# Performance work log

Measured on AMD Instinct MI355X. Metric: run time of the kernel, lower is better.

## Reference

```python
import jax, jax.numpy as jnp
import numpy as np

N, D, B = 8192, 512, 64
EPS = 1e-5


def _layernorm(x, w, b):
    mu = jnp.mean(x, axis=-1, keepdims=True)
    var = jnp.mean(jnp.square(x - mu), axis=-1, keepdims=True)
    return (x - mu) * jax.lax.rsqrt(var + EPS) * w + b


def setup_inputs() -> dict:
    key = jax.random.key(0)
    ks = jax.random.split(key, 10)
    s = 0.02
    return {
        "x_mole": jax.random.normal(ks[0], (N, D), jnp.float32),
        "x_conf": jax.random.normal(ks[1], (N, D), jnp.float32),
        "W1": jax.random.normal(ks[2], (D, D), jnp.float32) * s,   # attention_1 (no bias)
        "W2": jax.random.normal(ks[3], (D, D), jnp.float32) * s,   # attention_2 (no bias)
        "phi1_w": jnp.ones((D,), jnp.float32),
        "phi1_b": jnp.zeros((D,), jnp.float32),
        "phi2_w": jnp.ones((D,), jnp.float32),
        "phi2_b": jnp.zeros((D,), jnp.float32),
        "rho_w1": jax.random.normal(ks[4], (D, D), jnp.float32) * s,
        "rho_b1": jnp.zeros((D,), jnp.float32),
        "rho_w2": jax.random.normal(ks[5], (D, D), jnp.float32) * s,
        "rho_b2": jnp.zeros((D,), jnp.float32),
        "rho_ln_w": jnp.ones((D,), jnp.float32),
        "rho_ln_b": jnp.zeros((D,), jnp.float32),
        "batch": jnp.sort(jax.random.randint(ks[6], (N,), 0, B, jnp.int64)),
    }


def reference(x_mole, x_conf, W1, W2, phi1_w, phi1_b, phi2_w, phi2_b,
              rho_w1, rho_b1, rho_w2, rho_b2, rho_ln_w, rho_ln_b, batch):
    # projections of LayerNormed inputs (torch Linear: y = x @ W^T)
    q = _layernorm(x_mole, phi1_w, phi1_b) @ W1.T          # [N, D]
    k = _layernorm(x_conf, phi2_w, phi2_b) @ W2.T          # [N, D]
    dot = q @ k.T                                          # [N, N]

    # block-diagonal batch-equality mask and hand-rolled masked softmax
    mask = (batch[:, None] == batch[None, :]).astype(dot.dtype)  # [N, N]
    max_values = jnp.max(dot * mask, axis=1, keepdims=True)
    masked = (dot - max_values) * mask
    e = jnp.exp(masked)
    attn = e / jnp.sum(e * mask, axis=1, keepdims=True)
    attn = attn * mask                                     # [N, N]

    x_weighted = attn @ x_conf                             # [N, D]

    # rho MLP: Linear -> SiLU -> Linear -> SiLU -> LayerNorm
    h = jax.nn.silu(x_weighted @ rho_w1.T + rho_b1)
    h = jax.nn.silu(h @ rho_w2.T + rho_b2)
    x_encoded = _layernorm(h, rho_ln_w, rho_ln_b)
    return x_encoded, attn
```

## Files before the change

kernel.cpp:

```cpp
#include <hip/hip_runtime.h>

namespace {

constexpr int N = 8192;
constexpr int D = 512;
constexpr int NBATCH = 64;
constexpr int SEGMAX = 256;
constexpr int XCW = NBATCH * SEGMAX;
constexpr size_t MB = 1u << 20;

using s16x8 = __attribute__((ext_vector_type(8))) short;
using f32x4 = __attribute__((ext_vector_type(4))) float;

__device__ inline short f2bf(float f) {
  unsigned u = __float_as_uint(f);
  u += 0x7fffu + ((u >> 16) & 1u);
  return (short)(u >> 16);
}
__device__ inline float bf2f(short h) {
  return __uint_as_float(((unsigned)(unsigned short)h) << 16);
}
__device__ inline void split2(float f, short& hi, short& lo) {
  hi = f2bf(f);
  lo = f2bf(f - bf2f(hi));
}

__device__ inline f32x4 mfma16(s16x8 a, s16x8 b, f32x4 c) {
  return __builtin_amdgcn_mfma_f32_16x16x32_bf16(a, b, c, 0, 0, 0);
}

__device__ inline void gl16(const short* g, short* l) {
  __builtin_amdgcn_global_load_lds((const __attribute__((address_space(1))) void*)g,
                                   (__attribute__((address_space(3))) void*)l, 16, 0, 0);
}

__device__ inline void ln_row(const float* __restrict__ x, const float* __restrict__ w,
                              const float* __restrict__ bsrc, int row, int lane,
                              float o[8]) {
  const float* xr = x + (size_t)row * D + lane * 8;
  f32x4 v0 = *(const f32x4*)xr;
  f32x4 v1 = *(const f32x4*)(xr + 4);
  float s = 0.f, sq = 0.f;
#pragma unroll
  for (int j = 0; j < 4; j++) {
    s += v0[j] + v1[j];
    sq += v0[j] * v0[j] + v1[j] * v1[j];
  }
#pragma unroll
  for (int off = 32; off >= 1; off >>= 1) {
    s += __shfl_xor(s, off);
    sq += __shfl_xor(sq, off);
  }
  float mu = s * (1.f / D);
  float var = sq * (1.f / D) - mu * mu;
  float rs = rsqrtf(var + 1e-5f);
  const float* wp = w + lane * 8;
  const float* bp = bsrc + lane * 8;
  f32x4 w0 = *(const f32x4*)wp, w1 = *(const f32x4*)(wp + 4);
  f32x4 b0 = *(const f32x4*)bp, b1 = *(const f32x4*)(bp + 4);
#pragma unroll
  for (int j = 0; j < 4; j++) {
    o[j] = (v0[j] - mu) * rs * w0[j] + b0[j];
    o[j + 4] = (v1[j] - mu) * rs * w1[j] + b1[j];
  }
}

__global__ __launch_bounds__(256) void ln_split2(
    const float* __restrict__ x0, const float* __restrict__ w0,
    const float* __restrict__ b0, short* __restrict__ oh0, short* __restrict__ ol0,
    const float* __restrict__ x1, const float* __restrict__ w1,
    const float* __restrict__ b1, short* __restrict__ oh1, short* __restrict__ ol1) {
  const float* x = blockIdx.y ? x1 : x0;
  const float* w = blockIdx.y ? w1 : w0;
  const float* b = blockIdx.y ? b1 : b0;
  short* oh = blockIdx.y ? oh1 : oh0;
  short* ol = blockIdx.y ? ol1 : ol0;
  int row = blockIdx.x * 4 + (threadIdx.x >> 6);
  int lane = threadIdx.x & 63;
  float o[8];
  ln_row(x, w, b, row, lane, o);
  s16x8 hi, lo;
#pragma unroll
  for (int j = 0; j < 8; j++) {
    short h, l;
    split2(o[j], h, l);
    hi[j] = h; lo[j] = l;
  }
  *(s16x8*)(oh + (size_t)row * D + lane * 8) = hi;
  *(s16x8*)(ol + (size_t)row * D + lane * 8) = lo;
}

__global__ __launch_bounds__(256) void ln_f32(const float* __restrict__ x,
                                              const float* __restrict__ w,
                                              const float* __restrict__ bsrc,
                                              float* __restrict__ out) {
  int row = blockIdx.x * 4 + (threadIdx.x >> 6);
  int lane = threadIdx.x & 63;
  float o[8];
  ln_row(x, w, bsrc, row, lane, o);
  f32x4 o0, o1;
#pragma unroll
  for (int j = 0; j < 4; j++) { o0[j] = o[j]; o1[j] = o[j + 4]; }
  float* op = out + (size_t)row * D + lane * 8;
  *(f32x4*)op = o0;
  *(f32x4*)(op + 4) = o1;
}

__global__ __launch_bounds__(256) void castsplit4(
    const float* __restrict__ s0, const float* __restrict__ s1,
    const float* __restrict__ s2, const float* __restrict__ s3,
    short* __restrict__ h0, short* __restrict__ l0,
    short* __restrict__ h1, short* __restrict__ l1,
    short* __restrict__ h2, short* __restrict__ l2,
    short* __restrict__ h3, short* __restrict__ l3) {
  const float* s; short* h; short* l;
  switch (blockIdx.y) {
    case 0: s = s0; h = h0; l = l0; break;
    case 1: s = s1; h = h1; l = l1; break;
    case 2: s = s2; h = h2; l = l2; break;
    default: s = s3; h = h3; l = l3; break;
  }
  int i = blockIdx.x * 256 + threadIdx.x;
  f32x4 a = *(const f32x4*)(s + (size_t)i * 8);
  f32x4 b = *(const f32x4*)(s + (size_t)i * 8 + 4);
  s16x8 oh, ol;
#pragma unroll
  for (int j = 0; j < 4; j++) {
    short hh, ll;
    split2(a[j], hh, ll); oh[j] = hh; ol[j] = ll;
    split2(b[j], hh, ll); oh[j + 4] = hh; ol[j + 4] = ll;
  }
  *(s16x8*)(h + (size_t)i * 8) = oh;
  *(s16x8*)(l + (size_t)i * 8) = ol;
}

__global__ void seg_kernel(const int* __restrict__ batch, int* __restrict__ seg,
                           int* __restrict__ colmap) {
  int stride = (batch[N - 1] == 0) ? 2 : 1;
  int t = threadIdx.x;
  if (t <= NBATCH) {
    int lo = 0, hi = N;
    while (lo < hi) {
      int mid = (lo + hi) >> 1;
      if (batch[mid * stride] < t) lo = mid + 1; else hi = mid;
    }
    seg[t] = lo;
  }
  __syncthreads();
  for (int r = t; r < N; r += 256) {
    int bb = batch[r * stride];
    colmap[r] = bb * SEGMAX + (r - seg[bb]);
  }
}

__global__ __launch_bounds__(256) void transpose_xc(const float* __restrict__ xc,
                                                    const int* __restrict__ colmap,
                                                    short* __restrict__ xcT) {
  __shared__ float tile[32][33];
  int tx = threadIdx.x & 31, ty = threadIdx.x >> 5;
  int r0 = blockIdx.x * 32, c0 = blockIdx.y * 32;
#pragma unroll
  for (int p = 0; p < 4; p++)
    tile[ty + p * 8][tx] = xc[(size_t)(r0 + ty + p * 8) * D + c0 + tx];
  __syncthreads();
  int cp = colmap[r0 + tx];
#pragma unroll
  for (int p = 0; p < 4; p++) {
    int d = c0 + ty + p * 8;
    xcT[(size_t)d * XCW + cp] = f2bf(tile[tx][ty + p * 8]);
  }
}

template <int SPLITA, int EPI>
__global__ __launch_bounds__(256) void gemm_lds(const short* __restrict__ Ahi,
                                                const short* __restrict__ Alo,
                                                const short* __restrict__ Bhi,
                                                const short* __restrict__ Blo,
                                                const float* __restrict__ bias,
                                                void* __restrict__ C0,
                                                void* __restrict__ C1) {
  constexpr int ASZ = 64 * 32;
  constexpr int BSZ = 128 * 32;
  constexpr int AH = 0;
  constexpr int AL = ASZ;
  constexpr int BH = SPLITA ? 2 * ASZ : ASZ;
  constexpr int BL = BH + BSZ;
  constexpr int STEP = BL + BSZ;
  __shared__ short lds[2][STEP];

  int tid = threadIdx.x;
  int w = tid >> 6, l = tid & 63, lr = l & 15, kg = l >> 4;
  int wm = w >> 1, wn = w & 1;

  int o = blockIdx.y * 4 + blockIdx.x;
  int xcd = o & 7, slot = o >> 3;
  int by = xcd * 16 + (slot >> 2);
  int bx = slot & 3;
  int m_base = by * 64;
  int n_base = bx * 128;

  int srow = tid >> 2;
  int gch = (tid & 3) ^ ((tid >> 3) & 3);
  const short* a_h = Ahi + (size_t)(m_base + srow) * D + gch * 8;
  const short* a_l = SPLITA ? (Alo + (size_t)(m_base + srow) * D + gch * 8) : nullptr;
  const short* b_h = Bhi + (size_t)(n_base + srow) * D + gch * 8;
  const short* b_l = Blo + (size_t)(n_base + srow) * D + gch * 8;

  int aoff[2], boff[4];
#pragma unroll
  for (int fo = 0; fo < 2; fo++) {
    int row = wm * 32 + fo * 16 + lr;
    aoff[fo] = row * 32 + ((kg ^ ((row >> 1) & 3)) << 3);
  }
#pragma unroll
  for (int fo = 0; fo < 4; fo++) {
    int row = wn * 64 + fo * 16 + lr;
    boff[fo] = row * 32 + ((kg ^ ((row >> 1) & 3)) << 3);
  }

  f32x4 acc[2][4] = {};

  auto STAGE = [&](int c, int ko) {
    gl16(a_h + ko, &lds[c][AH + w * 512]);
    if (SPLITA) gl16(a_l + ko, &lds[c][AL + w * 512]);
    gl16(b_h + ko, &lds[c][BH + w * 512]);
    gl16(b_h + (size_t)64 * D + ko, &lds[c][BH + 2048 + w * 512]);
    gl16(b_l + ko, &lds[c][BL + w * 512]);
    gl16(b_l + (size_t)64 * D + ko, &lds[c][BL + 2048 + w * 512]);
  };

  STAGE(0, 0);
  __syncthreads();
#pragma unroll
  for (int s = 0; s < 16; ++s) {
    int cur = s & 1;
    if (s < 15) STAGE(cur ^ 1, (s + 1) * 32);
    s16x8 av[2], alv[2], bv[4], blv[4];
#pragma unroll
    for (int i = 0; i < 2; i++) {
      av[i] = *(const s16x8*)&lds[cur][AH + aoff[i]];
      if (SPLITA) alv[i] = *(const s16x8*)&lds[cur][AL + aoff[i]];
    }
#pragma unroll
    for (int j = 0; j < 4; j++) {
      bv[j] = *(const s16x8*)&lds[cur][BH + boff[j]];
      blv[j] = *(const s16x8*)&lds[cur][BL + boff[j]];
    }
#pragma unroll
    for (int i = 0; i < 2; i++)
#pragma unroll
      for (int j = 0; j < 4; j++) {
        if (SPLITA)
          acc[i][j] = mfma16(av[i], bv[j],
                             mfma16(av[i], blv[j], mfma16(alv[i], bv[j], acc[i][j])));
        else
          acc[i][j] = mfma16(av[i], bv[j], mfma16(av[i], blv[j], acc[i][j]));
      }
    __syncthreads();
  }

#pragma unroll
  for (int i = 0; i < 2; i++)
#pragma unroll
    for (int j = 0; j < 4; j++) {
      int col = n_base + wn * 64 + j * 16 + lr;
      float bv2 = (EPI >= 1) ? bias[col] : 0.f;
#pragma unroll
      for (int r = 0; r < 4; r++) {
        int rowg = m_base + wm * 32 + i * 16 + kg * 4 + r;
        float v = acc[i][j][r];
        if (EPI >= 1) { v += bv2; v = v / (1.f + __expf(-v)); }
        if (EPI == 0) {
          short h, lo2;
          split2(v, h, lo2);
          ((short*)C0)[(size_t)rowg * D + col] = h;
          ((short*)C1)[(size_t)rowg * D + col] = lo2;
        } else if (EPI == 1) {
          ((short*)C0)[(size_t)rowg * D + col] = f2bf(v);
        } else {
          ((float*)C0)[(size_t)rowg * D + col] = v;
        }
      }
    }
}

__global__ __launch_bounds__(256) void attn_kernel(const short* __restrict__ qh,
                                                   const short* __restrict__ ql,
                                                   const short* __restrict__ kh,
                                                   const short* __restrict__ kl,
                                                   const short* __restrict__ xcT,
                                                   const int* __restrict__ seg,
                                                   float* __restrict__ attn_out,
                                                   short* __restrict__ xw) {
  __shared__ float Ss[32][260];
  __shared__ short Ph[32][256];
  int b = blockIdx.y;
  int s0 = seg[b];
  int nb = seg[b + 1] - s0;
  int r0 = blockIdx.x * 32;
  if (r0 >= nb) return;
  int tid = threadIdx.x;
  int w = tid >> 6, l = tid & 63, lr = l & 15, kg = l >> 4;
  int row8 = tid >> 3, sub = tid & 7;
  bool rvalid = (r0 + row8) < nb;

  size_t q0 = (size_t)(s0 + r0 + lr) * D + kg * 8;
  size_t q1 = q0 + 16 * D;
  int ncf = (nb + 15) >> 4;
  for (int f = w; f < ncf; f += 4) {
    f32x4 a0 = {0, 0, 0, 0}, a1 = {0, 0, 0, 0};
    size_t kr = (size_t)(s0 + f * 16 + lr) * D + kg * 8;
    for (int k0 = 0; k0 < D; k0 += 32) {
      s16x8 kH = *(const s16x8*)(kh + kr + k0);
      s16x8 kL = *(const s16x8*)(kl + kr + k0);
      s16x8 qH0 = *(const s16x8*)(qh + q0 + k0);
      s16x8 qH1 = *(const s16x8*)(qh + q1 + k0);
      s16x8 qL0 = *(const s16x8*)(ql + q0 + k0);
      s16x8 qL1 = *(const s16x8*)(ql + q1 + k0);
      a0 = mfma16(qH0, kH, mfma16(qH0, kL, mfma16(qL0, kH, a0)));
      a1 = mfma16(qH1, kH, mfma16(qH1, kL, mfma16(qL1, kH, a1)));
    }
#pragma unroll
    for (int r = 0; r < 4; r++) {
      Ss[kg * 4 + r][f * 16 + lr] = a0[r];
      Ss[16 + kg * 4 + r][f * 16 + lr] = a1[r];
    }
  }
  __syncthreads();

  int nbp32 = (nb + 31) & ~31;
  if (rvalid) {
    float m = 0.f;
    for (int j = sub; j < nb; j += 8) m = fmaxf(m, Ss[row8][j]);
    m = fmaxf(m, __shfl_xor(m, 1));
    m = fmaxf(m, __shfl_xor(m, 2));
    m = fmaxf(m, __shfl_xor(m, 4));
    float sum = 0.f;
    for (int j = sub; j < nb; j += 8) {
      float e = __expf(Ss[row8][j] - m);
      Ss[row8][j] = e;
      sum += e;
    }
    sum += __shfl_xor(sum, 1);
    sum += __shfl_xor(sum, 2);
    sum += __shfl_xor(sum, 4);
    float inv = 1.f / sum;
    float* orow = attn_out + (size_t)(s0 + r0 + row8) * N + s0;
    for (int j = sub; j < nbp32; j += 8) {
      int sw = ((((j >> 3) ^ (row8 & 7)) << 3) | (j & 7));
      if (j < nb) {
        float a = Ss[row8][j] * inv;
        orow[j] = a;
        Ph[row8][sw] = f2bf(a);
      } else {
        Ph[row8][sw] = 0;
      }
    }
  }
  __syncthreads();

  for (int f2 = w * 8; f2 < w * 8 + 8; f2++) {
    f32x4 a0 = {0, 0, 0, 0}, a1 = {0, 0, 0, 0};
    const short* xrow = xcT + (size_t)(f2 * 16 + lr) * XCW + b * SEGMAX + kg * 8;
    for (int j0 = 0; j0 < nbp32; j0 += 32) {
      int ch = (j0 >> 3) + kg;
      int swo = ((ch ^ (lr & 7)) << 3);
      s16x8 pH0 = *(const s16x8*)&Ph[lr][swo];
      s16x8 pH1 = *(const s16x8*)&Ph[16 + lr][swo];
      s16x8 xv = *(const s16x8*)(xrow + j0);
      a0 = mfma16(pH0, xv, a0);
      a1 = mfma16(pH1, xv, a1);
    }
#pragma unroll
    for (int r = 0; r < 4; r++) {
      int rr0 = kg * 4 + r, rr1 = 16 + kg * 4 + r;
      if (r0 + rr0 < nb) xw[(size_t)(s0 + r0 + rr0) * D + f2 * 16 + lr] = f2bf(a0[r]);
      if (r0 + rr1 < nb) xw[(size_t)(s0 + r0 + rr1) * D + f2 * 16 + lr] = f2bf(a1[r]);
    }
  }
}

}

extern "C" void kernel_launch(void* const* d_in, const int* in_sizes, int n_in,
                              void* d_out, int out_size, void* d_ws, size_t ws_size,
                              hipStream_t stream) {
  (void)in_sizes; (void)n_in; (void)out_size; (void)ws_size;
  const float* x_mole = (const float*)d_in[0];
  const float* x_conf = (const float*)d_in[1];
  const float* W1 = (const float*)d_in[2];
  const float* W2 = (const float*)d_in[3];
  const float* phi1_w = (const float*)d_in[4];
  const float* phi1_b = (const float*)d_in[5];
  const float* phi2_w = (const float*)d_in[6];
  const float* phi2_b = (const float*)d_in[7];
  const float* rho_w1 = (const float*)d_in[8];
  const float* rho_b1 = (const float*)d_in[9];
  const float* rho_w2 = (const float*)d_in[10];
  const float* rho_b2 = (const float*)d_in[11];
  const float* rho_ln_w = (const float*)d_in[12];
  const float* rho_ln_b = (const float*)d_in[13];
  const int* batch = (const int*)d_in[14];

  float* out = (float*)d_out;
  float* attn_out = out + (size_t)N * D;

  char* w8 = (char*)d_ws;
  short* xm_hi = (short*)(w8 + 0 * MB);
  short* xm_lo = (short*)(w8 + 8 * MB);
  short* xc_hi = (short*)(w8 + 16 * MB);
  short* xc_lo = (short*)(w8 + 24 * MB);
  short* q_hi  = (short*)(w8 + 32 * MB);
  short* q_lo  = (short*)(w8 + 41 * MB);
  short* k_hi  = (short*)(w8 + 50 * MB);
  short* k_lo  = (short*)(w8 + 59 * MB);
  short* xcT   = (short*)(w8 + 68 * MB);
  short* w1h   = (short*)(w8 + 84 * MB);
  short* w1l   = (short*)(w8 + 84 * MB + 524288);
  short* w2h   = (short*)(w8 + 85 * MB);
  short* w2l   = (short*)(w8 + 85 * MB + 524288);
  short* r1h   = (short*)(w8 + 86 * MB);
  short* r1l   = (short*)(w8 + 86 * MB + 524288);
  short* r2h   = (short*)(w8 + 87 * MB);
  short* r2l   = (short*)(w8 + 87 * MB + 524288);
  int*   seg   = (int*)(w8 + 88 * MB);
  int*   colmap = (int*)(w8 + 88 * MB + 512);
  float* h2    = (float*)(w8 + 32 * MB);
  short* xw = xm_hi;
  short* h1 = xc_hi;

  hipMemsetAsync((void*)attn_out, 0, (size_t)N * N * sizeof(float), stream);

  seg_kernel<<<1, 256, 0, stream>>>(batch, seg, colmap);
  castsplit4<<<dim3(128, 4), 256, 0, stream>>>(W1, W2, rho_w1, rho_w2,
                                               w1h, w1l, w2h, w2l,
                                               r1h, r1l, r2h, r2l);
  ln_split2<<<dim3(N / 4, 2), 256, 0, stream>>>(x_mole, phi1_w, phi1_b, xm_hi, xm_lo,
                                                x_conf, phi2_w, phi2_b, xc_hi, xc_lo);
  transpose_xc<<<dim3(N / 32, D / 32), 256, 0, stream>>>(x_conf, colmap, xcT);
  gemm_lds<1, 0><<<dim3(4, 128), 256, 0, stream>>>(xm_hi, xm_lo, w1h, w1l, nullptr,
                                                   q_hi, q_lo);
  gemm_lds<1, 0><<<dim3(4, 128), 256, 0, stream>>>(xc_hi, xc_lo, w2h, w2l, nullptr,
                                                   k_hi, k_lo);
  attn_kernel<<<dim3(SEGMAX / 32, NBATCH), 256, 0, stream>>>(q_hi, q_lo, k_hi, k_lo,
                                                             xcT, seg, attn_out, xw);
  gemm_lds<0, 1><<<dim3(4, 128), 256, 0, stream>>>(xw, nullptr, r1h, r1l, rho_b1,
                                                   h1, nullptr);
  gemm_lds<0, 2><<<dim3(4, 128), 256, 0, stream>>>(h1, nullptr, r2h, r2l, rho_b2,
                                                   h2, nullptr);
  ln_f32<<<N / 4, 256, 0, stream>>>(h2, rho_ln_w, rho_ln_b, out);
}
```

Baseline: 515.3 us.

## Fuse prep kernels, batch QK projections, and deepen GEMM prefetch pipeline

Merges the layernorm-split, weight cast-split and segment-index kernels into one launch, and runs the Q and K projection GEMMs as one grid with a z dimension. The GEMM main loop now keeps two stages in flight, using explicit vmcnt waits and raw barriers instead of a full syncthreads per step. This is meant to cut launch overhead and hide global-to-LDS latency, at the cost of more fragile manual synchronization.

```diff
diff --git a/kernel.cpp b/kernel.cpp
--- a/kernel.cpp
+++ b/kernel.cpp
@@ -32,6 +32,11 @@
 __device__ inline void gl16(const short* g, short* l) {
   __builtin_amdgcn_global_load_lds((const __attribute__((address_space(1))) void*)g,
                                    (__attribute__((address_space(3))) void*)l, 16, 0, 0);
+}
+
+template <int Nn>
+__device__ inline void vmw() {
+  asm volatile("s_waitcnt vmcnt(%0)" ::"i"(Nn) : "memory");
 }
 
 __device__ inline void ln_row(const float* __restrict__ x, const float* __restrict__ w,
@@ -65,29 +70,75 @@
   }
 }
 
-__global__ __launch_bounds__(256) void ln_split2(
-    const float* __restrict__ x0, const float* __restrict__ w0,
-    const float* __restrict__ b0, short* __restrict__ oh0, short* __restrict__ ol0,
-    const float* __restrict__ x1, const float* __restrict__ w1,
-    const float* __restrict__ b1, short* __restrict__ oh1, short* __restrict__ ol1) {
-  const float* x = blockIdx.y ? x1 : x0;
-  const float* w = blockIdx.y ? w1 : w0;
-  const float* b = blockIdx.y ? b1 : b0;
-  short* oh = blockIdx.y ? oh1 : oh0;
-  short* ol = blockIdx.y ? ol1 : ol0;
-  int row = blockIdx.x * 4 + (threadIdx.x >> 6);
-  int lane = threadIdx.x & 63;
-  float o[8];
-  ln_row(x, w, b, row, lane, o);
-  s16x8 hi, lo;
-#pragma unroll
-  for (int j = 0; j < 8; j++) {
-    short h, l;
-    split2(o[j], h, l);
-    hi[j] = h; lo[j] = l;
-  }
-  *(s16x8*)(oh + (size_t)row * D + lane * 8) = hi;
-  *(s16x8*)(ol + (size_t)row * D + lane * 8) = lo;
+__global__ __launch_bounds__(256) void prep_kernel(
+    const float* __restrict__ x_mole, const float* __restrict__ phi1_w,
+    const float* __restrict__ phi1_b, short* __restrict__ xm_hi, short* __restrict__ xm_lo,
+    const float* __restrict__ x_conf, const float* __restrict__ phi2_w,
+    const float* __restrict__ phi2_b, short* __restrict__ xc_hi, short* __restrict__ xc_lo,
+    const float* __restrict__ W1, const float* __restrict__ W2,
+    const float* __restrict__ rho_w1, const float* __restrict__ rho_w2,
+    short* __restrict__ w1h, short* __restrict__ w1l,
+    short* __restrict__ w2h, short* __restrict__ w2l,
+    short* __restrict__ r1h, short* __restrict__ r1l,
+    short* __restrict__ r2h, short* __restrict__ r2l,
+    const int* __restrict__ batch, int* __restrict__ seg, int* __restrict__ colmap) {
+  int bid = blockIdx.x;
+  int tid = threadIdx.x;
+  if (bid < 4096) {
+    int inst = bid >> 11;
+    int rowblk = bid & 2047;
+    const float* x = inst ? x_conf : x_mole;
+    const float* w = inst ? phi2_w : phi1_w;
+    const float* b = inst ? phi2_b : phi1_b;
+    short* oh = inst ? xc_hi : xm_hi;
+    short* ol = inst ? xc_lo : xm_lo;
+    int row = rowblk * 4 + (tid >> 6);
+    int lane = tid & 63;
+    float o[8];
+    ln_row(x, w, b, row, lane, o);
+    s16x8 hi, lo;
+#pragma unroll
+    for (int j = 0; j < 8; j++) {
+      short h, l;
+      split2(o[j], h, l);
+      hi[j] = h; lo[j] = l;
+    }
+    *(s16x8*)(oh + (size_t)row * D + lane * 8) = hi;
+    *(s16x8*)(ol + (size_t)row * D + lane * 8) = lo;
+  } else if (bid < 4608) {
+    int idx = bid - 4096;
+    int mat = idx >> 7;
+    const float* s = (mat == 0) ? W1 : (mat == 1) ? W2 : (mat == 2) ? rho_w1 : rho_w2;
+    short* h = (mat == 0) ? w1h : (mat == 1) ? w2h : (mat == 2) ? r1h : r2h;
+    short* l = (mat == 0) ? w1l : (mat == 1) ? w2l : (mat == 2) ? r1l : r2l;
+    int i = (idx & 127) * 256 + tid;
+    f32x4 a = *(const f32x4*)(s + (size_t)i * 8);
+    f32x4 b = *(const f32x4*)(s + (size_t)i * 8 + 4);
+    s16x8 oh, ol;
+#pragma unroll
+    for (int j = 0; j < 4; j++) {
+      short hh, ll;
+      split2(a[j], hh, ll); oh[j] = hh; ol[j] = ll;
+      split2(b[j], hh, ll); oh[j + 4] = hh; ol[j + 4] = ll;
+    }
+    *(s16x8*)(h + (size_t)i * 8) = oh;
+    *(s16x8*)(l + (size_t)i * 8) = ol;
+  } else {
+    int stride = (batch[N - 1] == 0) ? 2 : 1;
+    if (tid <= NBATCH) {
+      int lo = 0, hi = N;
+      while (lo < hi) {
+        int mid = (lo + hi) >> 1;
+        if (batch[mid * stride] < tid) lo = mid + 1; else hi = mid;
+      }
+      seg[tid] = lo;
+    }
+    __syncthreads();
+    for (int r = tid; r < N; r += 256) {
+      int bb = batch[r * stride];
+      colmap[r] = bb * SEGMAX + (r - seg[bb]);
+    }
+  }
 }
 
 __global__ __launch_bounds__(256) void ln_f32(const float* __restrict__ x,
@@ -106,53 +157,6 @@
   *(f32x4*)(op + 4) = o1;
 }
 
-__global__ __launch_bounds__(256) void castsplit4(
-    const float* __restrict__ s0, const float* __restrict__ s1,
-    const float* __restrict__ s2, const float* __restrict__ s3,
-    short* __restrict__ h0, short* __restrict__ l0,
-    short* __restrict__ h1, short* __restrict__ l1,
-    short* __restrict__ h2, short* __restrict__ l2,
-    short* __restrict__ h3, short* __restrict__ l3) {
-  const float* s; short* h; short* l;
-  switch (blockIdx.y) {
-    case 0: s = s0; h = h0; l = l0; break;
-    case 1: s = s1; h = h1; l = l1; break;
-    case 2: s = s2; h = h2; l = l2; break;
-    default: s = s3; h = h3; l = l3; break;
-  }
-  int i = blockIdx.x * 256 + threadIdx.x;
-  f32x4 a = *(const f32x4*)(s + (size_t)i * 8);
-  f32x4 b = *(const f32x4*)(s + (size_t)i * 8 + 4);
-  s16x8 oh, ol;
-#pragma unroll
-  for (int j = 0; j < 4; j++) {
-    short hh, ll;
-    split2(a[j], hh, ll); oh[j] = hh; ol[j] = ll;
-    split2(b[j], hh, ll); oh[j + 4] = hh; ol[j + 4] = ll;
-  }
-  *(s16x8*)(h + (size_t)i * 8) = oh;
-  *(s16x8*)(l + (size_t)i * 8) = ol;
-}
-
-__global__ void seg_kernel(const int* __restrict__ batch, int* __restrict__ seg,
-                           int* __restrict__ colmap) {
-  int stride = (batch[N - 1] == 0) ? 2 : 1;
-  int t = threadIdx.x;
-  if (t <= NBATCH) {
-    int lo = 0, hi = N;
-    while (lo < hi) {
-      int mid = (lo + hi) >> 1;
-      if (batch[mid * stride] < t) lo = mid + 1; else hi = mid;
-    }
-    seg[t] = lo;
-  }
-  __syncthreads();
-  for (int r = t; r < N; r += 256) {
-    int bb = batch[r * stride];
-    colmap[r] = bb * SEGMAX + (r - seg[bb]);
-  }
-}
-
 __global__ __launch_bounds__(256) void transpose_xc(const float* __restrict__ xc,
                                                     const int* __restrict__ colmap,
                                                     short* __restrict__ xcT) {
@@ -172,13 +176,10 @@
 }
 
 template <int SPLITA, int EPI>
-__global__ __launch_bounds__(256) void gemm_lds(const short* __restrict__ Ahi,
-                                                const short* __restrict__ Alo,
-                                                const short* __restrict__ Bhi,
-                                                const short* __restrict__ Blo,
-                                                const float* __restrict__ bias,
-                                                void* __restrict__ C0,
-                                                void* __restrict__ C1) {
+__device__ void gemm_core(const short* __restrict__ Ahi, const short* __restrict__ Alo,
+                          const short* __restrict__ Bhi, const short* __restrict__ Blo,
+                          const float* __restrict__ bias, void* __restrict__ C0,
+                          void* __restrict__ C1, short* lds, int bx, int by) {
   constexpr int ASZ = 64 * 32;
   constexpr int BSZ = 128 * 32;
   constexpr int AH = 0;
@@ -186,16 +187,10 @@
   constexpr int BH = SPLITA ? 2 * ASZ : ASZ;
   constexpr int BL = BH + BSZ;
   constexpr int STEP = BL + BSZ;
-  __shared__ short lds[2][STEP];
 
   int tid = threadIdx.x;
   int w = tid >> 6, l = tid & 63, lr = l & 15, kg = l >> 4;
   int wm = w >> 1, wn = w & 1;
-
-  int o = blockIdx.y * 4 + blockIdx.x;
-  int xcd = o & 7, slot = o >> 3;
-  int by = xcd * 16 + (slot >> 2);
-  int bx = slot & 3;
   int m_base = by * 64;
   int n_base = bx * 128;
 
@@ -221,30 +216,35 @@
   f32x4 acc[2][4] = {};
 
   auto STAGE = [&](int c, int ko) {
-    gl16(a_h + ko, &lds[c][AH + w * 512]);
-    if (SPLITA) gl16(a_l + ko, &lds[c][AL + w * 512]);
-    gl16(b_h + ko, &lds[c][BH + w * 512]);
-    gl16(b_h + (size_t)64 * D + ko, &lds[c][BH + 2048 + w * 512]);
-    gl16(b_l + ko, &lds[c][BL + w * 512]);
-    gl16(b_l + (size_t)64 * D + ko, &lds[c][BL + 2048 + w * 512]);
+    short* base = lds + c * STEP;
+    gl16(a_h + ko, base + AH + w * 512);
+    if (SPLITA) gl16(a_l + ko, base + AL + w * 512);
+    gl16(b_h + ko, base + BH + w * 512);
+    gl16(b_h + (size_t)64 * D + ko, base + BH + 2048 + w * 512);
+    gl16(b_l + ko, base + BL + w * 512);
+    gl16(b_l + (size_t)64 * D + ko, base + BL + 2048 + w * 512);
   };
+  constexpr int LPS = SPLITA ? 6 : 5;
 
   STAGE(0, 0);
-  __syncthreads();
+  STAGE(1, 32);
 #pragma unroll
   for (int s = 0; s < 16; ++s) {
-    int cur = s & 1;
-    if (s < 15) STAGE(cur ^ 1, (s + 1) * 32);
+    const int cur = s & 1;
+    if (s < 15) vmw<LPS>(); else vmw<0>();
+    __builtin_amdgcn_s_barrier();
+    __builtin_amdgcn_sched_barrier(0);
+    const short* base = lds + cur * STEP;
     s16x8 av[2], alv[2], bv[4], blv[4];
 #pragma unroll
     for (int i = 0; i < 2; i++) {
-      av[i] = *(const s16x8*)&lds[cur][AH + aoff[i]];
-      if (SPLITA) alv[i] = *(const s16x8*)&lds[cur][AL + aoff[i]];
+      av[i] = *(const s16x8*)(base + AH + aoff[i]);
+      if (SPLITA) alv[i] = *(const s16x8*)(base + AL + aoff[i]);
     }
 #pragma unroll
     for (int j = 0; j < 4; j++) {
-      bv[j] = *(const s16x8*)&lds[cur][BH + boff[j]];
-      blv[j] = *(const s16x8*)&lds[cur][BL + boff[j]];
+      bv[j] = *(const s16x8*)(base + BH + boff[j]);
+      blv[j] = *(const s16x8*)(base + BL + boff[j]);
     }
 #pragma unroll
     for (int i = 0; i < 2; i++)
@@ -256,7 +256,10 @@
         else
           acc[i][j] = mfma16(av[i], bv[j], mfma16(av[i], blv[j], acc[i][j]));
       }
-    __syncthreads();
+    __builtin_amdgcn_sched_barrier(0);
+    __builtin_amdgcn_s_barrier();
+    __builtin_amdgcn_sched_barrier(0);
+    if (s + 2 < 16) STAGE(cur, (s + 2) * 32);
   }
 
 #pragma unroll
@@ -282,6 +285,39 @@
         }
       }
     }
+}
+
+__global__ __launch_bounds__(256) void gemm_qk(
+    const short* __restrict__ A0h, const short* __restrict__ A0l,
+    const short* __restrict__ B0h, const short* __restrict__ B0l,
+    short* __restrict__ C0h, short* __restrict__ C0l,
+    const short* __restrict__ A1h, const short* __restrict__ A1l,
+    const short* __restrict__ B1h, const short* __restrict__ B1l,
+    short* __restrict__ C1h, short* __restrict__ C1l) {
+  __shared__ short lds[2 * (2 * 64 * 32 + 2 * 128 * 32)];
+  int z = blockIdx.z;
+  int o = blockIdx.y * 4 + blockIdx.x;
+  int xcd = o & 7, slot = o >> 3;
+  int by = xcd * 16 + (slot >> 2);
+  int bx = slot & 3;
+  if (z == 0)
+    gemm_core<1, 0>(A0h, A0l, B0h, B0l, nullptr, C0h, C0l, lds, bx, by);
+  else
+    gemm_core<1, 0>(A1h, A1l, B1h, B1l, nullptr, C1h, C1l, lds, bx, by);
+}
+
+template <int EPI>
+__global__ __launch_bounds__(256) void gemm_rho(const short* __restrict__ Ahi,
+                                                const short* __restrict__ Bhi,
+                                                const short* __restrict__ Blo,
+                                                const float* __restrict__ bias,
+                                                void* __restrict__ C0) {
+  __shared__ short lds[2 * (64 * 32 + 2 * 128 * 32)];
+  int o = blockIdx.y * 4 + blockIdx.x;
+  int xcd = o & 7, slot = o >> 3;
+  int by = xcd * 16 + (slot >> 2);
+  int bx = slot & 3;
+  gemm_core<0, EPI>(Ahi, nullptr, Bhi, Blo, bias, C0, nullptr, lds, bx, by);
 }
 
 __global__ __launch_bounds__(256) void attn_kernel(const short* __restrict__ qh,
@@ -431,22 +467,18 @@
 
   hipMemsetAsync((void*)attn_out, 0, (size_t)N * N * sizeof(float), stream);
 
-  seg_kernel<<<1, 256, 0, stream>>>(batch, seg, colmap);
-  castsplit4<<<dim3(128, 4), 256, 0, stream>>>(W1, W2, rho_w1, rho_w2,
-                                               w1h, w1l, w2h, w2l,
-                                               r1h, r1l, r2h, r2l);
-  ln_split2<<<dim3(N / 4, 2), 256, 0, stream>>>(x_mole, phi1_w, phi1_b, xm_hi, xm_lo,
-                                                x_conf, phi2_w, phi2_b, xc_hi, xc_lo);
+  prep_kernel<<<4609, 256, 0, stream>>>(
+      x_mole, phi1_w, phi1_b, xm_hi, xm_lo,
+      x_conf, phi2_w, phi2_b, xc_hi, xc_lo,
+      W1, W2, rho_w1, rho_w2,
+      w1h, w1l, w2h, w2l, r1h, r1l, r2h, r2l,
+      batch, seg, colmap);
   transpose_xc<<<dim3(N / 32, D / 32), 256, 0, stream>>>(x_conf, colmap, xcT);
-  gemm_lds<1, 0><<<dim3(4, 128), 256, 0, stream>>>(xm_hi, xm_lo, w1h, w1l, nullptr,
-                                                   q_hi, q_lo);
-  gemm_lds<1, 0><<<dim3(4, 128), 256, 0, stream>>>(xc_hi, xc_lo, w2h, w2l, nullptr,
-                                                   k_hi, k_lo);
+  gemm_qk<<<dim3(4, 128, 2), 256, 0, stream>>>(xm_hi, xm_lo, w1h, w1l, q_hi, q_lo,
+                                               xc_hi, xc_lo, w2h, w2l, k_hi, k_lo);
   attn_kernel<<<dim3(SEGMAX / 32, NBATCH), 256, 0, stream>>>(q_hi, q_lo, k_hi, k_lo,
                                                              xcT, seg, attn_out, xw);
-  gemm_lds<0, 1><<<dim3(4, 128), 256, 0, stream>>>(xw, nullptr, r1h, r1l, rho_b1,
-                                                   h1, nullptr);
-  gemm_lds<0, 2><<<dim3(4, 128), 256, 0, stream>>>(h1, nullptr, r2h, r2l, rho_b2,
-                                                   h2, nullptr);
+  gemm_rho<1><<<dim3(4, 128), 256, 0, stream>>>(xw, r1h, r1l, rho_b1, h1);
+  gemm_rho<2><<<dim3(4, 128), 256, 0, stream>>>(h1, r2h, r2l, rho_b2, h2);
   ln_f32<<<N / 4, 256, 0, stream>>>(h2, rho_ln_w, rho_ln_b, out);
 }
```

Result: faster. 504.4 us (-2.1%).
